# Performance work log

Hardware: AMD Instinct MI355X
Metric: run time of the kernel (lower is better)

## Reference

```python
import math
import jax, jax.numpy as jnp
import numpy as np

D_MODEL = 768
EXPAND = 2
D_INNER = EXPAND * D_MODEL  # 1536
D_STATE = 16
D_CONV = 4
DT_RANK = math.ceil(D_INNER / 16)  # 96
B, L = 2, 2048
LN_EPS = 1e-5


def setup_inputs() -> dict:
    key = jax.random.key(0)
    ks = jax.random.split(key, 10)
    x = jax.random.normal(ks[0], (B, L, D_MODEL), dtype=jnp.float32)
    ln_g = jnp.ones((D_MODEL,), jnp.float32)
    ln_b = jnp.zeros((D_MODEL,), jnp.float32)
    W_in = jax.random.normal(ks[1], (D_MODEL, 2 * D_INNER), jnp.float32) / np.sqrt(D_MODEL)
    conv_w = jax.random.normal(ks[2], (D_INNER, 1, D_CONV), jnp.float32) / np.sqrt(D_CONV)
    conv_b = jax.random.normal(ks[3], (D_INNER,), jnp.float32) * 0.02
    W_xproj = jax.random.normal(ks[4], (D_INNER, DT_RANK + 2 * D_STATE), jnp.float32) / np.sqrt(D_INNER)
    W_dt = jax.random.normal(ks[5], (DT_RANK, D_INNER), jnp.float32) / np.sqrt(DT_RANK)
    # dt bias init: inverse-softplus of dt ~ LogUniform(1e-3, 1e-1)
    dt = jnp.exp(jax.random.uniform(ks[6], (D_INNER,)) * (math.log(0.1) - math.log(0.001)) + math.log(0.001))
    b_dt = dt + jnp.log(-jnp.expm1(-dt))
    log_A = jnp.log(jnp.tile(jnp.arange(1, D_STATE + 1, dtype=jnp.float32), (D_INNER, 1)))  # (d_inner, N)
    D_param = jnp.ones((D_INNER,), jnp.float32)
    W_out = jax.random.normal(ks[7], (D_INNER, D_MODEL), jnp.float32) / np.sqrt(D_INNER)
    return dict(x=x, ln_g=ln_g, ln_b=ln_b, W_in=W_in, conv_w=conv_w, conv_b=conv_b,
                W_xproj=W_xproj, W_dt=W_dt, b_dt=b_dt, log_A=log_A, D_param=D_param, W_out=W_out)


def _mamba_block(x, ln_g, ln_b, W_in, conv_w, conv_b, W_xproj, W_dt, b_dt, log_A, D_param, W_out):
    residual = x
    # LayerNorm
    mu = jnp.mean(x, axis=-1, keepdims=True)
    var = jnp.var(x, axis=-1, keepdims=True)
    xn = (x - mu) * jax.lax.rsqrt(var + LN_EPS) * ln_g + ln_b
    # in projection -> (u, v)
    uv = xn @ W_in  # (B, L, 2*d_inner)
    u, v = jnp.split(uv, 2, axis=-1)
    # causal depthwise conv1d along length (torch pads both sides then truncates -> left pad only)
    u_c = jnp.transpose(u, (0, 2, 1))  # (B, d_inner, L)
    u_c = jax.lax.conv_general_dilated(
        u_c, conv_w, window_strides=(1,), padding=[(D_CONV - 1, 0)],
        dimension_numbers=('NCH', 'OIH', 'NCH'), feature_group_count=D_INNER)
    u_c = u_c + conv_b[None, :, None]
    u = jnp.transpose(u_c, (0, 2, 1))  # (B, L, d_inner)
    u = jax.nn.silu(u)
    # Selective SSM
    x_dbl = u @ W_xproj  # (B, L, dt_rank + 2N)
    dlt, Bm, Cm = jnp.split(x_dbl, [DT_RANK, DT_RANK + D_STATE], axis=-1)
    delta = jax.nn.softplus(dlt @ W_dt + b_dt)  # (B, L, d_inner)
    A = -jnp.exp(log_A)  # (d_inner, N)
    A_bar = jnp.exp(jnp.einsum('bld,dn->bldn', delta, A))         # discretized A
    Bu = jnp.einsum('bld,bln,bld->bldn', delta, Bm, u)            # B_bar * u
    # parallel scan: h_k = A_bar_k * h_{k-1} + Bu_k
    def comb(e1, e2):
        a1, b1 = e1
        a2, b2 = e2
        return a1 * a2, a2 * b1 + b2
    _, h = jax.lax.associative_scan(comb, (A_bar, Bu), axis=1)
    y = jnp.einsum('bldn,bln->bld', h, Cm) + u * D_param
    # gate + residual
    y = y * jax.nn.silu(v)
    return y @ W_out + residual


def reference(x, ln_g, ln_b, W_in, conv_w, conv_b, W_xproj, W_dt, b_dt, log_A, D_param, W_out):
    return _mamba_block(x, ln_g, ln_b, W_in, conv_w, conv_b, W_xproj, W_dt, b_dt, log_A, D_param, W_out)
```

## Files before the change

### kernel.cpp

```cpp
#include <hip/hip_runtime.h>

#define D_MODEL 768
#define D_INNER 1536
#define D_STATE 16
#define DT_RANK 96
#define BB 2
#define LL 2048
#define TT (BB*LL)
#define NC 64
#define CL 32
#define SKK 4
#define LOG2E 1.44269504f

typedef unsigned short u16;
typedef short bf16x8 __attribute__((ext_vector_type(8)));
typedef unsigned short u16x8 __attribute__((ext_vector_type(8)));
typedef float f32x4  __attribute__((ext_vector_type(4)));

__device__ __forceinline__ float bf2f(u16 u) {
    union { unsigned int i; float f; } c; c.i = ((unsigned int)u) << 16; return c.f;
}
__device__ __forceinline__ u16 f2bf(float f) {
    union { float f; unsigned int i; } c; c.f = f;
    unsigned int x = c.i;
    return (u16)((x + 0x7fffu + ((x >> 16) & 1u)) >> 16);
}
__device__ __forceinline__ float bfu_lo(unsigned int u) {
    union { unsigned int i; float f; } c; c.i = u << 16; return c.f;
}
__device__ __forceinline__ float bfu_hi(unsigned int u) {
    union { unsigned int i; float f; } c; c.i = u & 0xFFFF0000u; return c.f;
}
__device__ __forceinline__ float ldx(const void* p, size_t i, bool f32) {
    return f32 ? ((const float*)p)[i] : bf2f(((const u16*)p)[i]);
}

__device__ __forceinline__ void gload16(const u16* g, u16* l) {
    __builtin_amdgcn_global_load_lds(
        (const __attribute__((address_space(1))) unsigned int*)g,
        (__attribute__((address_space(3))) unsigned int*)l, 16, 0, 0);
}

__device__ __forceinline__ void xcd_swz(int& bx, int& by) {
    const int gx = gridDim.x;
    const int cpx = (gx * gridDim.y) >> 3;
    const int bid = by * gx + bx;
    const int w = (bid & 7) * cpx + (bid >> 3);
    bx = w % gx; by = w / gx;
}

__global__ void detect_kernel(const void* x, int* flag)
{
    __shared__ int bad;
    if (threadIdx.x == 0) bad = 0;
    __syncthreads();
    const u16* p = (const u16*)x;
    int local = 0;
    for (int i = threadIdx.x; i < 2048; i += 256) {
        const float v = bf2f(p[2 * i]);
        if (!(fabsf(v) < 1e4f)) local = 1;
    }
    if (local) atomicOr(&bad, 1);
    __syncthreads();
    if (threadIdx.x == 0) *flag = bad;
}

__global__ __launch_bounds__(256) void prep_kernel(
    const void* __restrict__ W_in, const void* __restrict__ W_xp,
    const void* __restrict__ W_dt, const void* __restrict__ W_out,
    u16* __restrict__ WtIn, u16* __restrict__ WtXp,
    u16* __restrict__ WtDt, u16* __restrict__ WtOut,
    const void* __restrict__ x, const void* __restrict__ g,
    const void* __restrict__ b, u16* __restrict__ xn,
    const int* __restrict__ flagp)
{
    const bool f32 = (*flagp != 0);
    int bid = blockIdx.x;
    const int t = threadIdx.x;
    if (bid >= 960) {
        const int tok = bid - 960;
        const size_t base = (size_t)tok * D_MODEL;
        float v[3];
        v[0] = ldx(x, base + t, f32);
        v[1] = ldx(x, base + t + 256, f32);
        v[2] = ldx(x, base + t + 512, f32);
        float s = v[0] + v[1] + v[2];
        float q = v[0]*v[0] + v[1]*v[1] + v[2]*v[2];
        #pragma unroll
        for (int o = 32; o > 0; o >>= 1) {
            s += __shfl_down(s, o, 64);
            q += __shfl_down(q, o, 64);
        }
        __shared__ float ss[4], qq[4];
        if ((t & 63) == 0) { ss[t >> 6] = s; qq[t >> 6] = q; }
        __syncthreads();
        const float S = ss[0] + ss[1] + ss[2] + ss[3];
        const float Q = qq[0] + qq[1] + qq[2] + qq[3];
        const float mu  = S * (1.f / D_MODEL);
        const float var = Q * (1.f / D_MODEL) - mu * mu;
        const float rs  = rsqrtf(var + 1e-5f);
        u16* outr = xn + base;
        #pragma unroll
        for (int i = 0; i < 3; ++i) {
            const int c = t + i * 256;
            outr[c] = f2bf((v[i] - mu) * rs * ldx(g, c, f32) + ldx(b, c, f32));
        }
        return;
    }
    const void* src; u16* dst; int K, N, bx, by;
    if (bid < 576)      { src = W_in;  dst = WtIn;  K = 768;  N = 3072; bx = bid % 48; by = bid / 48; }
    else if (bid < 624) { bid -= 576; src = W_xp;  dst = WtXp;  K = 1536; N = 128;  bx = bid % 2;  by = bid / 2; }
    else if (bid < 672) { bid -= 624; src = W_dt;  dst = WtDt;  K = 96;   N = 1536; bx = bid % 24; by = bid / 24; }
    else                { bid -= 672; src = W_out; dst = WtOut; K = 1536; N = 768;  bx = bid % 12; by = bid / 12; }
    __shared__ u16 tile[64][72];
    const int n0 = bx * 64, k0 = by * 64;
    {
        const int r = t >> 2, c = (t & 3) * 16;
        const int k = k0 + r;
        if (k < K) {
            if (f32) {
                const float* sp = (const float*)src + (size_t)k * N + n0 + c;
                #pragma unroll
                for (int q = 0; q < 4; ++q) {
                    const float4 v = *(const float4*)(sp + 4 * q);
                    tile[r][c + 4*q + 0] = f2bf(v.x);
                    tile[r][c + 4*q + 1] = f2bf(v.y);
                    tile[r][c + 4*q + 2] = f2bf(v.z);
                    tile[r][c + 4*q + 3] = f2bf(v.w);
                }
            } else {
                const u16* sp = (const u16*)src + (size_t)k * N + n0 + c;
                *(u16x8*)(&tile[r][c])     = *(const u16x8*)(sp);
                *(u16x8*)(&tile[r][c + 8]) = *(const u16x8*)(sp + 8);
            }
        }
    }
    __syncthreads();
    {
        const int nl = t >> 2, kl = (t & 3) * 16;
        const int n = n0 + nl;
        if (k0 + kl < K) {
            u16x8 t0, t1;
            #pragma unroll
            for (int i = 0; i < 8; ++i) t0[i] = tile[kl + i][nl];
            #pragma unroll
            for (int i = 0; i < 8; ++i) t1[i] = tile[kl + 8 + i][nl];
            u16* dp = dst + (size_t)n * K + k0 + kl;
            *(u16x8*)(dp)     = t0;
            *(u16x8*)(dp + 8) = t1;
        }
    }
}

template<int EPI, int BK>
__global__ __launch_bounds__(256) void mfma_gemm(
    const u16* __restrict__ A, const u16* __restrict__ Bt,
    u16* __restrict__ C, void* __restrict__ Cout, const void* __restrict__ aux,
    float* __restrict__ Cf, const int* __restrict__ flagp,
    int Kslice, int lda, int ldbt, int ldc)
{
    const bool f32 = (*flagp != 0);
    __shared__ alignas(16) u16 As[3 * 64 * BK];
    __shared__ alignas(16) u16 Bs[3 * 64 * BK];
    const int tid  = threadIdx.x;
    const int wave = tid >> 6, lane = tid & 63;
    const int lrow = lane & 15, quad = lane >> 4;
    int bx = blockIdx.x, by = blockIdx.y;
    if (gridDim.z == 1) xcd_swz(bx, by);
    const int row0 = by * 64, col0 = bx * 64;
    const int k0   = blockIdx.z * Kslice;
    constexpr int LPR = BK / 8;
    constexpr int RPO = 64 / LPR;
    constexpr int NOP = BK / 32;
    constexpr int V1  = 2 * NOP;
    constexpr int V2  = 4 * NOP;
    const int srow = lane / LPR;
    const int skk  = (lane % LPR) * 8;
    const int wb   = wave * 16 * BK;
    const u16* gA = A  + (size_t)(row0 + wave * 16 + srow) * lda  + k0 + skk;
    const u16* gB = Bt + (size_t)(col0 + wave * 16 + srow) * ldbt + k0 + skk;
    const int nst = Kslice / BK;
    constexpr int BUF = 64 * BK;
    #pragma unroll
    for (int o = 0; o < NOP; ++o) {
        gload16(gA + (size_t)o * RPO * lda,  &As[wb + o * 512]);
        gload16(gB + (size_t)o * RPO * ldbt, &Bs[wb + o * 512]);
    }
    if (nst > 1) {
        #pragma unroll
        for (int o = 0; o < NOP; ++o) {
            gload16(gA + BK + (size_t)o * RPO * lda,  &As[BUF + wb + o * 512]);
            gload16(gB + BK + (size_t)o * RPO * ldbt, &Bs[BUF + wb + o * 512]);
        }
    }
    f32x4 acc[4] = {{0.f,0.f,0.f,0.f},{0.f,0.f,0.f,0.f},{0.f,0.f,0.f,0.f},{0.f,0.f,0.f,0.f}};
    int cur = 0, nxt2 = 2;
    for (int t = 0; t < nst; ++t) {
        if (t + 2 < nst) {
            const int kt = (t + 2) * BK;
            const int poff = nxt2 * BUF;
            #pragma unroll
            for (int o = 0; o < NOP; ++o) {
                gload16(gA + kt + (size_t)o * RPO * lda,  &As[poff + wb + o * 512]);
                gload16(gB + kt + (size_t)o * RPO * ldbt, &Bs[poff + wb + o * 512]);
            }
            asm volatile("s_waitcnt vmcnt(%0)" :: "i"(V2) : "memory");
        } else if (t + 1 < nst) {
            asm volatile("s_waitcnt vmcnt(%0)" :: "i"(V1) : "memory");
        } else {
            asm volatile("s_waitcnt vmcnt(0)" ::: "memory");
        }
        __builtin_amdgcn_s_barrier();
        asm volatile("" ::: "memory");
        const int boff = cur * BUF;
        #pragma unroll
        for (int kk = 0; kk < NOP; ++kk) {
            const bf16x8 af = *(const bf16x8*)(&As[boff + (wave * 16 + lrow) * BK + kk * 32 + quad * 8]);
            #pragma unroll
            for (int q = 0; q < 4; ++q) {
                const bf16x8 bq = *(const bf16x8*)(&Bs[boff + (q * 16 + lrow) * BK + kk * 32 + quad * 8]);
                acc[q] = __builtin_amdgcn_mfma_f32_16x16x32_bf16(af, bq, acc[q], 0, 0, 0);
            }
        }
        __builtin_amdgcn_s_barrier();
        asm volatile("" ::: "memory");
        cur = (cur == 2) ? 0 : cur + 1;
        nxt2 = (nxt2 == 2) ? 0 : nxt2 + 1;
    }
    #pragma unroll
    for (int t = 0; t < 4; ++t) {
        #pragma unroll
        for (int r = 0; r < 4; ++r) {
            const int row = row0 + wave * 16 + quad * 4 + r;
            const int col = col0 + t * 16 + lrow;
            const size_t idx = (size_t)row * ldc + col;
            float vv = acc[t][r];
            if (EPI == 1) {
                vv += ldx(aux, col, f32);
                vv = (vv > 20.f) ? vv : log1pf(__expf(vv));
                C[idx] = f2bf(vv);
            } else if (EPI == 2) {
                vv += ldx(aux, idx, f32);
                if (f32) ((float*)Cout)[idx] = vv;
                else     ((u16*)Cout)[idx]   = f2bf(vv);
            } else if (EPI == 3) {
                atomicAdd(&Cf[idx], vv);
            } else {
                C[idx] = f2bf(vv);
            }
        }
    }
}

template<int EPI>
__global__ __launch_bounds__(256) void mfma_gemm128(
    const u16* __restrict__ A, const u16* __restrict__ Bt,
    u16* __restrict__ C, void* __restrict__ Cout, const void* __restrict__ aux,
    const int* __restrict__ flagp,
    int K, int lda, int ldbt, int ldc)
{
    const bool f32 = (*flagp != 0);
    __shared__ alignas(16) u16 As[3 * 128 * 32];
    __shared__ alignas(16) u16 Bs[3 * 128 * 32];
    const int tid  = threadIdx.x;
    const int wave = tid >> 6, lane = tid & 63;
    const int lrow = lane & 15, quad = lane >> 4;
    const int wy = wave >> 1, wx = wave & 1;
    int bx = blockIdx.x, by = blockIdx.y;
    if (gridDim.z == 1) xcd_swz(bx, by);
    const int row0 = by * 128, col0 = bx * 128;
    const int skk = (lane & 3) * 8;
    const int r0 = wave * 16 + (lane >> 2);
    const int r1 = r0 + 64;
    const int wb0 = wave * 512, wb1 = (wave + 4) * 512;
    const u16* gA0 = A  + (size_t)(row0 + r0) * lda  + skk;
    const u16* gA1 = A  + (size_t)(row0 + r1) * lda  + skk;
    const u16* gB0 = Bt + (size_t)(col0 + r0) * ldbt + skk;
    const u16* gB1 = Bt + (size_t)(col0 + r1) * ldbt + skk;
    const int nst = K >> 5;
    constexpr int BUF = 128 * 32;
    gload16(gA0, &As[wb0]); gload16(gA1, &As[wb1]);
    gload16(gB0, &Bs[wb0]); gload16(gB1, &Bs[wb1]);
    if (nst > 1) {
        gload16(gA0 + 32, &As[BUF + wb0]); gload16(gA1 + 32, &As[BUF + wb1]);
        gload16(gB0 + 32, &Bs[BUF + wb0]); gload16(gB1 + 32, &Bs[BUF + wb1]);
    }
    f32x4 acc[4][4];
    #pragma unroll
    for (int i = 0; i < 4; ++i)
        #pragma unroll
        for (int j = 0; j < 4; ++j) acc[i][j] = (f32x4){0.f,0.f,0.f,0.f};
    int cur = 0, nxt2 = 2;
    for (int t = 0; t < nst; ++t) {
        if (t + 2 < nst) {
            const int kt = (t + 2) * 32;
            const int poff = nxt2 * BUF;
            gload16(gA0 + kt, &As[poff + wb0]); gload16(gA1 + kt, &As[poff + wb1]);
            gload16(gB0 + kt, &Bs[poff + wb0]); gload16(gB1 + kt, &Bs[poff + wb1]);
            asm volatile("s_waitcnt vmcnt(8)" ::: "memory");
        } else if (t + 1 < nst) {
            asm volatile("s_waitcnt vmcnt(4)" ::: "memory");
        } else {
            asm volatile("s_waitcnt vmcnt(0)" ::: "memory");
        }
        __builtin_amdgcn_s_barrier();
        asm volatile("" ::: "memory");
        const int boff = cur * BUF;
        bf16x8 af[4], bf_[4];
        #pragma unroll
        for (int i = 0; i < 4; ++i)
            af[i] = *(const bf16x8*)(&As[boff + (wy * 64 + i * 16 + lrow) * 32 + quad * 8]);
        #pragma unroll
        for (int j = 0; j < 4; ++j)
            bf_[j] = *(const bf16x8*)(&Bs[boff + (wx * 64 + j * 16 + lrow) * 32 + quad * 8]);
        #pragma unroll
        for (int i = 0; i < 4; ++i)
            #pragma unroll
            for (int j = 0; j < 4; ++j)
                acc[i][j] = __builtin_amdgcn_mfma_f32_16x16x32_bf16(af[i], bf_[j], acc[i][j], 0, 0, 0);
        __builtin_amdgcn_s_barrier();
        asm volatile("" ::: "memory");
        cur = (cur == 2) ? 0 : cur + 1;
        nxt2 = (nxt2 == 2) ? 0 : nxt2 + 1;
    }
    #pragma unroll
    for (int i = 0; i < 4; ++i) {
        #pragma unroll
        for (int j = 0; j < 4; ++j) {
            #pragma unroll
            for (int r = 0; r < 4; ++r) {
                const int row = row0 + wy * 64 + i * 16 + quad * 4 + r;
                const int col = col0 + wx * 64 + j * 16 + lrow;
                const size_t idx = (size_t)row * ldc + col;
                float vv = acc[i][j][r];
                if (EPI == 1) {
                    vv += ldx(aux, col, f32);
                    vv = (vv > 20.f) ? vv : log1pf(__expf(vv));
                    C[idx] = f2bf(vv);
                } else if (EPI == 2) {
                    vv += ldx(aux, idx, f32);
                    if (f32) ((float*)Cout)[idx] = vv;
                    else     ((u16*)Cout)[idx]   = f2bf(vv);
                } else {
                    C[idx] = f2bf(vv);
                }
            }
        }
    }
}

__global__ __launch_bounds__(256) void convert_kernel(const float* __restrict__ src,
                                                      u16* __restrict__ dst, int n)
{
    const int i = blockIdx.x * 256 + threadIdx.x;
    if (i < n) dst[i] = f2bf(src[i]);
}

__global__ __launch_bounds__(256) void conv_silu_kernel(
    const u16* __restrict__ uv, const void* __restrict__ cw, const void* __restrict__ cb,
    u16* __restrict__ us, const int* __restrict__ flagp)
{
    const bool f32 = (*flagp != 0);
    const int gid = blockIdx.x * 256 + threadIdx.x;
    const int nd8 = D_INNER / 8;
    const int d8  = gid % nd8;
    const int tok = gid / nd8;
    const int d   = d8 * 8;
    const int l   = tok & (LL - 1);
    float acc[8], w[4][8];
    #pragma unroll
    for (int i = 0; i < 8; ++i) acc[i] = ldx(cb, d + i, f32);
    #pragma unroll
    for (int i = 0; i < 8; ++i) {
        if (f32) {
            const float4 wv = *(const float4*)((const float*)cw + (size_t)(d + i) * 4);
            w[0][i] = wv.x; w[1][i] = wv.y; w[2][i] = wv.z; w[3][i] = wv.w;
        } else {
            const u16* wp = (const u16*)cw + (size_t)(d + i) * 4;
            w[0][i] = bf2f(wp[0]); w[1][i] = bf2f(wp[1]);
            w[2][i] = bf2f(wp[2]); w[3][i] = bf2f(wp[3]);
        }
    }
    #pragma unroll
    for (int j = 0; j < 4; ++j) {
        if (l - 3 + j >= 0) {
            const u16x8 uvv = *(const u16x8*)(&uv[(size_t)(tok - 3 + j) * (2 * D_INNER) + d]);
            #pragma unroll
            for (int i = 0; i < 8; ++i) acc[i] += bf2f(uvv[i]) * w[j][i];
        }
    }
    u16x8 o;
    #pragma unroll
    for (int i = 0; i < 8; ++i) o[i] = f2bf(acc[i] / (1.f + __expf(-acc[i])));
    *(u16x8*)(&us[(size_t)tok * D_INNER + d]) = o;
}

__global__ __launch_bounds__(256) void scan1_kernel(
    const u16* __restrict__ delta, const u16* __restrict__ us,
    const u16* __restrict__ xdbl, const void* __restrict__ log_A,
    float* __restrict__ carrySD, float* __restrict__ carryH,
    const int* __restrict__ flagp)
{
    const bool f32 = (*flagp != 0);
    const int d = blockIdx.x * 256 + threadIdx.x;
    const int c = blockIdx.y, b = blockIdx.z;
    float A2[16], h[16];
    #pragma unroll
    for (int j = 0; j < 16; ++j) {
        A2[j] = -__expf(ldx(log_A, d * D_STATE + j, f32)) * LOG2E;
        h[j] = 0.f;
    }
    bool pw = true;
    #pragma unroll
    for (int j = 1; j < 16; ++j)
        pw = pw && (fabsf(A2[j] - (j + 1) * A2[0]) <= 0.02f * (j + 1) * fabsf(A2[0]));
    float sdl = 0.f;
    size_t tok = (size_t)b * LL + c * CL;
    if (pw) {
        #pragma unroll 2
        for (int t = 0; t < CL; ++t, ++tok) {
            const float dl = bf2f(delta[tok * D_INNER + d]);
            const float ul = bf2f(us[tok * D_INNER + d]);
            const uint4 B0 = *(const uint4*)(xdbl + tok * 128 + DT_RANK);
            const uint4 B1 = *(const uint4*)(xdbl + tok * 128 + DT_RANK + 8);
            const float dlul = dl * ul;
            sdl += dl;
            const unsigned int bw[8] = {B0.x,B0.y,B0.z,B0.w,B1.x,B1.y,B1.z,B1.w};
            const float a1 = exp2f(dl * A2[0]);
            float aj = 1.f;
            #pragma unroll
            for (int j = 0; j < 16; ++j) {
                aj *= a1;
                const float Bn = (j & 1) ? bfu_hi(bw[j >> 1]) : bfu_lo(bw[j >> 1]);
                h[j] = aj * h[j] + dlul * Bn;
            }
        }
    } else {
        #pragma unroll 2
        for (int t = 0; t < CL; ++t, ++tok) {
            const float dl = bf2f(delta[tok * D_INNER + d]);
            const float ul = bf2f(us[tok * D_INNER + d]);
            const uint4 B0 = *(const uint4*)(xdbl + tok * 128 + DT_RANK);
            const uint4 B1 = *(const uint4*)(xdbl + tok * 128 + DT_RANK + 8);
            const float dlul = dl * ul;
            sdl += dl;
            const unsigned int bw[8] = {B0.x,B0.y,B0.z,B0.w,B1.x,B1.y,B1.z,B1.w};
            #pragma unroll
            for (int j = 0; j < 16; ++j) {
                const float Bn = (j & 1) ? bfu_hi(bw[j >> 1]) : bfu_lo(bw[j >> 1]);
                h[j] = exp2f(dl * A2[j]) * h[j] + dlul * Bn;
            }
        }
    }
    const size_t cc = (size_t)b * NC + c;
    carrySD[cc * D_INNER + d] = sdl;
    const size_t ci = cc * (D_INNER * D_STATE) + d;
    #pragma unroll
    for (int j = 0; j < 16; ++j)
        carryH[ci + (size_t)j * D_INNER] = h[j];
}

__global__ __launch_bounds__(256) void scan2_kernel(
    const float* __restrict__ carrySD, float* __restrict__ carryH,
    const void* __restrict__ log_A, const int* __restrict__ flagp)
{
    const bool f32 = (*flagp != 0);
    const int gid = blockIdx.x * 256 + threadIdx.x;
    const int b   = gid / (D_INNER * D_STATE);
    const int dn  = gid % (D_INNER * D_STATE);
    const int j   = dn / D_INNER, d = dn % D_INNER;
    const float A2j = -__expf(ldx(log_A, d * D_STATE + j, f32)) * LOG2E;
    float hrun = 0.f;
    #pragma unroll 4
    for (int c = 0; c < NC; ++c) {
        const size_t cc = (size_t)b * NC + c;
        const float sdl = carrySD[cc * D_INNER + d];
        const size_t ci = cc * (D_INNER * D_STATE) + dn;
        const float hh = carryH[ci];
        carryH[ci] = hrun;
        hrun = exp2f(A2j * sdl) * hrun + hh;
    }
}

__global__ __launch_bounds__(256) void scan3_kernel(
    const u16* __restrict__ delta, const u16* __restrict__ us,
    const u16* __restrict__ xdbl, u16* __restrict__ uv,
    const void* __restrict__ log_A, const void* __restrict__ D_param,
    const float* __restrict__ carryH, const int* __restrict__ flagp)
{
    const bool f32 = (*flagp != 0);
    const int d = blockIdx.x * 256 + threadIdx.x;
    const int c = blockIdx.y, b = blockIdx.z;
    const float Dd = ldx(D_param, d, f32);
    float A2[16], h[16];
    const size_t ci = ((size_t)b * NC + c) * (D_INNER * D_STATE) + d;
    #pragma unroll
    for (int j = 0; j < 16; ++j)
        A2[j] = -__expf(ldx(log_A, d * D_STATE + j, f32)) * LOG2E;
    bool pw = true;
    #pragma unroll
    for (int j = 1; j < 16; ++j)
        pw = pw && (fabsf(A2[j] - (j + 1) * A2[0]) <= 0.02f * (j + 1) * fabsf(A2[0]));
    #pragma unroll
    for (int j = 0; j < 16; ++j)
        h[j] = carryH[ci + (size_t)j * D_INNER];
    size_t tok = (size_t)b * LL + c * CL;
    if (pw) {
        #pragma unroll 2
        for (int t = 0; t < CL; ++t, ++tok) {
            const float dl = bf2f(delta[tok * D_INNER + d]);
            const float ul = bf2f(us[tok * D_INNER + d]);
            const uint4 B0 = *(const uint4*)(xdbl + tok * 128 + DT_RANK);
            const uint4 B1 = *(const uint4*)(xdbl + tok * 128 + DT_RANK + 8);
            const uint4 C0 = *(const uint4*)(xdbl + tok * 128 + DT_RANK + D_STATE);
            const uint4 C1 = *(const uint4*)(xdbl + tok * 128 + DT_RANK + D_STATE + 8);
            const float dlul = dl * ul;
            const unsigned int bw[8] = {B0.x,B0.y,B0.z,B0.w,B1.x,B1.y,B1.z,B1.w};
            const unsigned int cw_[8] = {C0.x,C0.y,C0.z,C0.w,C1.x,C1.y,C1.z,C1.w};
            const float a1 = exp2f(dl * A2[0]);
            float aj = 1.f, p = 0.f;
            #pragma unroll
            for (int j = 0; j < 16; ++j) {
                aj *= a1;
                const float Bn = (j & 1) ? bfu_hi(bw[j >> 1]) : bfu_lo(bw[j >> 1]);
                const float Cn = (j & 1) ? bfu_hi(cw_[j >> 1]) : bfu_lo(cw_[j >> 1]);
                h[j] = aj * h[j] + dlul * Bn;
                p += h[j] * Cn;
            }
            const float vv = bf2f(uv[tok * (2*D_INNER) + D_INNER + d]);
            uv[tok * (2*D_INNER) + d] = f2bf((p + ul * Dd) * (vv / (1.f + __expf(-vv))));
        }
    } else {
        #pragma unroll 2
        for (int t = 0; t < CL; ++t, ++tok) {
            const float dl = bf2f(delta[tok * D_INNER + d]);
            const float ul = bf2f(us[tok * D_INNER + d]);
            const uint4 B0 = *(const uint4*)(xdbl + tok * 128 + DT_RANK);
            const uint4 B1 = *(const uint4*)(xdbl + tok * 128 + DT_RANK + 8);
            const uint4 C0 = *(const uint4*)(xdbl + tok * 128 + DT_RANK + D_STATE);
            const uint4 C1 = *(const uint4*)(xdbl + tok * 128 + DT_RANK + D_STATE + 8);
            const float dlul = dl * ul;
            const unsigned int bw[8] = {B0.x,B0.y,B0.z,B0.w,B1.x,B1.y,B1.z,B1.w};
            const unsigned int cw_[8] = {C0.x,C0.y,C0.z,C0.w,C1.x,C1.y,C1.z,C1.w};
            float p = 0.f;
            #pragma unroll
            for (int j = 0; j < 16; ++j) {
                const float Bn = (j & 1) ? bfu_hi(bw[j >> 1]) : bfu_lo(bw[j >> 1]);
                const float Cn = (j & 1) ? bfu_hi(cw_[j >> 1]) : bfu_lo(cw_[j >> 1]);
                h[j] = exp2f(dl * A2[j]) * h[j] + dlul * Bn;
                p += h[j] * Cn;
            }
            const float vv = bf2f(uv[tok * (2*D_INNER) + D_INNER + d]);
            uv[tok * (2*D_INNER) + d] = f2bf((p + ul * Dd) * (vv / (1.f + __expf(-vv))));
        }
    }
}

extern "C" void kernel_launch(void* const* d_in, const int* in_sizes, int n_in,
                              void* d_out, int out_size, void* d_ws, size_t ws_size,
                              hipStream_t stream)
{
    const void* x      = d_in[0];
    const void* ln_g   = d_in[1];
    const void* ln_b   = d_in[2];
    const void* W_in   = d_in[3];
    const void* conv_w = d_in[4];
    const void* conv_b = d_in[5];
    const void* W_xp   = d_in[6];
    const void* W_dt   = d_in[7];
    const void* b_dt   = d_in[8];
    const void* log_A  = d_in[9];
    const void* D_par  = d_in[10];
    const void* W_out  = d_in[11];

    int* flag  = (int*)d_ws;
    u16* ws    = (u16*)((char*)d_ws + 512);
    u16* xn    = ws;
    u16* uv    = xn + (size_t)TT * D_MODEL;
    u16* us    = uv + (size_t)TT * 2 * D_INNER;
    u16* xdbl  = us + (size_t)TT * D_INNER;
    u16* delta = xdbl + (size_t)TT * 128;
    float* carryH  = (float*)(delta + (size_t)TT * D_INNER);
    float* carrySD = carryH + (size_t)BB * NC * D_INNER * D_STATE;
    u16* WtIn  = (u16*)(carrySD + (size_t)BB * NC * D_INNER);
    u16* WtXp  = WtIn  + (size_t)2 * D_INNER * D_MODEL;
    u16* WtDt  = WtXp  + (size_t)(DT_RANK + 2 * D_STATE) * D_INNER;
    u16* WtOut = WtDt  + (size_t)D_INNER * DT_RANK;
    float* xdblF = (float*)(WtOut + (size_t)D_MODEL * D_INNER);

    detect_kernel<<<1, 256, 0, stream>>>(x, flag);
    hipMemsetAsync(xdblF, 0, (size_t)TT * 128 * sizeof(float), stream);
    prep_kernel<<<960 + TT, 256, 0, stream>>>(
        W_in, W_xp, W_dt, W_out, WtIn, WtXp, WtDt, WtOut,
        x, ln_g, ln_b, xn, flag);
    mfma_gemm128<0><<<dim3(2 * D_INNER / 128, TT / 128), 256, 0, stream>>>(
        xn, WtIn, uv, nullptr, nullptr, flag, D_MODEL, D_MODEL, D_MODEL, 2 * D_INNER);
    conv_silu_kernel<<<(TT * D_INNER / 8) / 256, 256, 0, stream>>>(uv, conv_w, conv_b, us, flag);
    mfma_gemm<3, 64><<<dim3(2, TT / 64, SKK), 256, 0, stream>>>(
        us, WtXp, nullptr, nullptr, nullptr, xdblF, flag,
        D_INNER / SKK, D_INNER, D_INNER, 128);
    convert_kernel<<<(TT * 128 + 255) / 256, 256, 0, stream>>>(xdblF, xdbl, TT * 128);
    mfma_gemm<1, 32><<<dim3(D_INNER / 64, TT / 64, 1), 256, 0, stream>>>(
        xdbl, WtDt, delta, nullptr, b_dt, nullptr, flag,
        DT_RANK, 128, DT_RANK, D_INNER);
    scan1_kernel<<<dim3(D_INNER / 256, NC, BB), 256, 0, stream>>>(
        delta, us, xdbl, log_A, carrySD, carryH, flag);
    scan2_kernel<<<(BB * D_INNER * D_STATE) / 256, 256, 0, stream>>>(
        carrySD, carryH, log_A, flag);
    scan3_kernel<<<dim3(D_INNER / 256, NC, BB), 256, 0, stream>>>(
        delta, us, xdbl, uv, log_A, D_par, carryH, flag);
    mfma_gemm<2, 64><<<dim3(D_MODEL / 64, TT / 64, 1), 256, 0, stream>>>(
        uv, WtOut, nullptr, d_out, x, nullptr, flag,
        D_INNER, 2 * D_INNER, D_INNER, D_MODEL);
}
```

Before: 291.3 us.

## Fold dtype detection into prep, swizzle LDS tiles, replace split-K atomics with partial buffers

Moves the input-dtype detection into every prep_kernel block so the separate detect launch disappears, and drops the memset. The split-K GEMM now writes per-slice partial results to separate buffers, and the convert kernel sums them, instead of doing atomicAdd into a zeroed buffer. Both GEMM kernels apply an XOR swizzle on the LDS column chunk to reduce bank conflicts on the fragment reads. The trade-offs are redundant detection reads in every prep block, extra workspace for four partial slices, and extra reads in the convert kernel.

```diff
diff --git a/kernel.cpp b/kernel.cpp
--- a/kernel.cpp
+++ b/kernel.cpp
@@ -49,22 +49,6 @@
     bx = w % gx; by = w / gx;
 }
 
-__global__ void detect_kernel(const void* x, int* flag)
-{
-    __shared__ int bad;
-    if (threadIdx.x == 0) bad = 0;
-    __syncthreads();
-    const u16* p = (const u16*)x;
-    int local = 0;
-    for (int i = threadIdx.x; i < 2048; i += 256) {
-        const float v = bf2f(p[2 * i]);
-        if (!(fabsf(v) < 1e4f)) local = 1;
-    }
-    if (local) atomicOr(&bad, 1);
-    __syncthreads();
-    if (threadIdx.x == 0) *flag = bad;
-}
-
 __global__ __launch_bounds__(256) void prep_kernel(
     const void* __restrict__ W_in, const void* __restrict__ W_xp,
     const void* __restrict__ W_dt, const void* __restrict__ W_out,
@@ -72,11 +56,23 @@
     u16* __restrict__ WtDt, u16* __restrict__ WtOut,
     const void* __restrict__ x, const void* __restrict__ g,
     const void* __restrict__ b, u16* __restrict__ xn,
-    const int* __restrict__ flagp)
-{
-    const bool f32 = (*flagp != 0);
+    int* __restrict__ flagw)
+{
+    const int t = threadIdx.x;
+    __shared__ int sbad;
+    if (t == 0) sbad = 0;
+    __syncthreads();
+    {
+        const u16* px = (const u16*)x;
+        int bad = 0;
+        for (int i = t; i < 2048; i += 256)
+            if (!(fabsf(bf2f(px[2 * i])) < 1e4f)) bad = 1;
+        if (bad) atomicOr(&sbad, 1);
+    }
+    __syncthreads();
+    const bool f32 = (sbad != 0);
     int bid = blockIdx.x;
-    const int t = threadIdx.x;
+    if (bid == 0 && t == 0) *flagw = sbad;
     if (bid >= 960) {
         const int tok = bid - 960;
         const size_t base = (size_t)tok * D_MODEL;
@@ -170,12 +166,14 @@
     const int row0 = by * 64, col0 = bx * 64;
     const int k0   = blockIdx.z * Kslice;
     constexpr int LPR = BK / 8;
+    constexpr int PM  = LPR - 1;
     constexpr int RPO = 64 / LPR;
     constexpr int NOP = BK / 32;
     constexpr int V1  = 2 * NOP;
     constexpr int V2  = 4 * NOP;
     const int srow = lane / LPR;
-    const int skk  = (lane % LPR) * 8;
+    const int pc   = (lane % LPR) ^ (srow & PM);
+    const int skk  = pc * 8;
     const int wb   = wave * 16 * BK;
     const u16* gA = A  + (size_t)(row0 + wave * 16 + srow) * lda  + k0 + skk;
     const u16* gB = Bt + (size_t)(col0 + wave * 16 + srow) * ldbt + k0 + skk;
@@ -194,6 +192,7 @@
         }
     }
     f32x4 acc[4] = {{0.f,0.f,0.f,0.f},{0.f,0.f,0.f,0.f},{0.f,0.f,0.f,0.f},{0.f,0.f,0.f,0.f}};
+    const int sw = (lrow & PM) << 3;
     int cur = 0, nxt2 = 2;
     for (int t = 0; t < nst; ++t) {
         if (t + 2 < nst) {
@@ -215,10 +214,12 @@
         const int boff = cur * BUF;
         #pragma unroll
         for (int kk = 0; kk < NOP; ++kk) {
-            const bf16x8 af = *(const bf16x8*)(&As[boff + (wave * 16 + lrow) * BK + kk * 32 + quad * 8]);
+            const bf16x8 af = *(const bf16x8*)(
+                &As[boff + (wave * 16 + lrow) * BK + ((kk * 32 + quad * 8) ^ sw)]);
             #pragma unroll
             for (int q = 0; q < 4; ++q) {
-                const bf16x8 bq = *(const bf16x8*)(&Bs[boff + (q * 16 + lrow) * BK + kk * 32 + quad * 8]);
+                const bf16x8 bq = *(const bf16x8*)(
+                    &Bs[boff + (q * 16 + lrow) * BK + ((kk * 32 + quad * 8) ^ sw)]);
                 acc[q] = __builtin_amdgcn_mfma_f32_16x16x32_bf16(af, bq, acc[q], 0, 0, 0);
             }
         }
@@ -244,7 +245,7 @@
                 if (f32) ((float*)Cout)[idx] = vv;
                 else     ((u16*)Cout)[idx]   = f2bf(vv);
             } else if (EPI == 3) {
-                atomicAdd(&Cf[idx], vv);
+                Cf[(size_t)blockIdx.z * (TT * 128) + idx] = vv;
             } else {
                 C[idx] = f2bf(vv);
             }
@@ -269,8 +270,10 @@
     int bx = blockIdx.x, by = blockIdx.y;
     if (gridDim.z == 1) xcd_swz(bx, by);
     const int row0 = by * 128, col0 = bx * 128;
-    const int skk = (lane & 3) * 8;
-    const int r0 = wave * 16 + (lane >> 2);
+    const int srw = lane >> 2;
+    const int pc  = (lane & 3) ^ (srw & 3);
+    const int skk = pc * 8;
+    const int r0 = wave * 16 + srw;
     const int r1 = r0 + 64;
     const int wb0 = wave * 512, wb1 = (wave + 4) * 512;
     const u16* gA0 = A  + (size_t)(row0 + r0) * lda  + skk;
@@ -290,6 +293,7 @@
     for (int i = 0; i < 4; ++i)
         #pragma unroll
         for (int j = 0; j < 4; ++j) acc[i][j] = (f32x4){0.f,0.f,0.f,0.f};
+    const int sw = (lrow & 3) << 3;
     int cur = 0, nxt2 = 2;
     for (int t = 0; t < nst; ++t) {
         if (t + 2 < nst) {
@@ -309,10 +313,12 @@
         bf16x8 af[4], bf_[4];
         #pragma unroll
         for (int i = 0; i < 4; ++i)
-            af[i] = *(const bf16x8*)(&As[boff + (wy * 64 + i * 16 + lrow) * 32 + quad * 8]);
+            af[i] = *(const bf16x8*)(
+                &As[boff + (wy * 64 + i * 16 + lrow) * 32 + ((quad * 8) ^ sw)]);
         #pragma unroll
         for (int j = 0; j < 4; ++j)
-            bf_[j] = *(const bf16x8*)(&Bs[boff + (wx * 64 + j * 16 + lrow) * 32 + quad * 8]);
+            bf_[j] = *(const bf16x8*)(
+                &Bs[boff + (wx * 64 + j * 16 + lrow) * 32 + ((quad * 8) ^ sw)]);
         #pragma unroll
         for (int i = 0; i < 4; ++i)
             #pragma unroll
@@ -353,7 +359,8 @@
                                                       u16* __restrict__ dst, int n)
 {
     const int i = blockIdx.x * 256 + threadIdx.x;
-    if (i < n) dst[i] = f2bf(src[i]);
+    if (i < n)
+        dst[i] = f2bf(src[i] + src[i + TT*128] + src[i + 2*TT*128] + src[i + 3*TT*128]);
 }
 
 __global__ __launch_bounds__(256) void conv_silu_kernel(
@@ -588,8 +595,6 @@
     u16* WtOut = WtDt  + (size_t)D_INNER * DT_RANK;
     float* xdblF = (float*)(WtOut + (size_t)D_MODEL * D_INNER);
 
-    detect_kernel<<<1, 256, 0, stream>>>(x, flag);
-    hipMemsetAsync(xdblF, 0, (size_t)TT * 128 * sizeof(float), stream);
     prep_kernel<<<960 + TT, 256, 0, stream>>>(
         W_in, W_xp, W_dt, W_out, WtIn, WtXp, WtDt, WtOut,
         x, ln_g, ln_b, xn, flag);
```

New measurement: 280.3 us. -3.8%, faster.
